# Kernel tuning notes

Hardware: AMD Instinct MI355X
Metric: run time of the kernel (lower is better)

Reference implementation:

```python
import jax, jax.numpy as jnp
import numpy as np

N = 50000      # nodes
E = 800000     # edges
FEAT = 128     # input feature dim
EMB = 256      # embed_dim = heads * hid
H = 4          # attention heads
C = 64         # hid_dim per head
PED = 32       # positional encoding dim
NEG_SLOPE = 0.2


def setup_inputs() -> dict:
    key = jax.random.key(0)
    ks = jax.random.split(key, 20)
    s = lambda i, shape, sc=0.1: jax.random.normal(ks[i], shape, jnp.float32) * sc
    return {
        "x": s(0, (N, FEAT), 1.0),
        "x_masked": s(1, (N, FEAT), 1.0),
        "PE": s(2, (N, PED), 1.0),
        "PE_noise": s(3, (N, PED), 1.0),
        "edge_index": jax.random.randint(ks[4], (2, E), 0, N),
        # PEG positional encoder (linear + relu)
        "W_peg": s(5, (PED, PED)), "b_peg": jnp.zeros((PED,), jnp.float32),
        # GAT layer 0
        "W0": s(6, (FEAT, H * C)), "a_s0": s(7, (H, C)), "a_d0": s(8, (H, C)),
        "w_pe0": s(9, (H,)), "W_u0": s(10, (PED, PED)),
        # GAT layer 1
        "W1": s(11, (EMB, H * C)), "a_s1": s(12, (H, C)), "a_d1": s(13, (H, C)),
        "w_pe1": s(14, (H,)), "W_u1": s(15, (PED, PED)),
    }


def _gat(x, pe, src, dst, W, a_s, a_d, w_pe, W_u):
    # PE-aware GATConv: standard GAT attention + PE-distance bias per head.
    xp = (x @ W).reshape(-1, H, C)                       # [N,H,C]
    al_s = (xp * a_s).sum(-1)                            # [N,H]
    al_d = (xp * a_d).sum(-1)                            # [N,H]
    dist = jnp.sqrt(((pe[src] - pe[dst]) ** 2).sum(-1) + 1e-8)   # [E]
    logits = jax.nn.leaky_relu(al_s[src] + al_d[dst], NEG_SLOPE) \
             + dist[:, None] * w_pe                      # [E,H]
    # segment softmax over incoming edges of each dst node
    m = jax.ops.segment_max(logits, dst, num_segments=N)
    e = jnp.exp(logits - m[dst])
    den = jax.ops.segment_sum(e, dst, num_segments=N)
    alpha = e / (den[dst] + 1e-16)                       # [E,H]
    out = jax.ops.segment_sum(alpha[:, :, None] * xp[src], dst,
                              num_segments=N).reshape(-1, H * C)  # [N,H*C]
    pe_out = jax.nn.relu(pe @ W_u)                       # per-layer PE update
    return out, pe_out


def reference(x, x_masked, PE, PE_noise, W_peg, b_peg,
              W0, a_s0, a_d0, w_pe0, W_u0,
              W1, a_s1, a_d1, w_pe1, W_u1, edge_index):
    src, dst = edge_index[0], edge_index[1]
    # PEG encoder on both PE branches
    pe = jax.nn.relu(PE @ W_peg + b_peg)
    pe_n = jax.nn.relu(PE_noise @ W_peg + b_peg)
    # layer 0 (dual branches; eval mode -> dropout is identity)
    h, pe_n = _gat(x, pe_n, src, dst, W0, a_s0, a_d0, w_pe0, W_u0)
    hm, pe = _gat(x_masked, pe, src, dst, W0, a_s0, a_d0, w_pe0, W_u0)
    h = jax.nn.relu(h)
    hm = jax.nn.relu(hm)
    # layer 1 (last layer: no activation)
    h, pe_n = _gat(h, pe_n, src, dst, W1, a_s1, a_d1, w_pe1, W_u1)
    hm, pe = _gat(hm, pe, src, dst, W1, a_s1, a_d1, w_pe1, W_u1)
    return (hm, pe_n)
```

## Files before the change

### kernel.cpp

```cpp
#include <hip/hip_runtime.h>
#include <hip/hip_bf16.h>

#define N_NODES 50000
#define N_EDGES 800000
#define NEG_SLOPE 0.2f

typedef __hip_bfloat16 bf16;
typedef __attribute__((ext_vector_type(8))) short short8;
typedef __attribute__((ext_vector_type(4))) float f32x4;
typedef __attribute__((ext_vector_type(2))) float f32x2;

__device__ __forceinline__ float b2f(bf16 x) { return __bfloat162float(x); }

__device__ __forceinline__ float ldsel(const void* p, size_t i, int isbf) {
  return isbf ? __bfloat162float(((const bf16*)p)[i]) : ((const float*)p)[i];
}
__device__ __forceinline__ void stsel(void* p, size_t i, int isbf, float v) {
  if (isbf) ((bf16*)p)[i] = __float2bfloat16(v);
  else ((float*)p)[i] = v;
}

__device__ __forceinline__ int block_detect(const unsigned short* __restrict__ probe) {
  __shared__ int wcount;
  int tid = threadIdx.x;
  if (tid == 0) wcount = 0;
  __syncthreads();
  int ex = (probe[2 * tid] >> 7) & 0xFF;
  unsigned long long m = __ballot(ex >= 0x85);
  if ((tid & 63) == 0) atomicAdd(&wcount, __popcll(m));
  __syncthreads();
  return wcount < 8;
}

struct CvtJobs {
  const void* src[10];
  float* dst[10];
  int n[10];
};
__global__ __launch_bounds__(256) void prep_kernel(CvtJobs jobs,
                                                   const unsigned short* __restrict__ probe,
                                                   const void* __restrict__ W0in,
                                                   bf16* __restrict__ Wt0,
                                                   const void* __restrict__ W1in,
                                                   bf16* __restrict__ Wt1,
                                                   int* __restrict__ flag,
                                                   const int* __restrict__ dst,
                                                   int* __restrict__ deg) {
  int tid = threadIdx.x;
  int b = blockIdx.x;
  if (b >= 400) {
    int e = (b - 400) * 256 + tid;
    atomicAdd(&deg[dst[e]], 1);
    return;
  }
  int isbf = block_detect(probe);
  if (b == 0 && tid == 0) *flag = isbf;
  if (b < 16) {
    for (int j = 0; j < 10; j++) {
      int n = jobs.n[j];
      const void* s = jobs.src[j];
      float* d = jobs.dst[j];
      for (int i = b * 256 + tid; i < n; i += 16 * 256) d[i] = ldsel(s, i, isbf);
    }
  } else if (b < 16 + 128) {
    int i = (b - 16) * 256 + tid;
    int n = i >> 7, k = i & 127;
    Wt0[i] = __float2bfloat16(ldsel(W0in, (size_t)k * 256 + n, isbf));
  } else {
    int i = (b - 144) * 256 + tid;
    int n = i >> 8, k = i & 255;
    Wt1[i] = __float2bfloat16(ldsel(W1in, (size_t)k * 256 + n, isbf));
  }
}

__global__ __launch_bounds__(1024) void scan_kernel(const int* __restrict__ deg,
                                                    int* __restrict__ rowptr,
                                                    int* __restrict__ bsum,
                                                    int* __restrict__ flags, int n) {
  __shared__ int wsum[16];
  __shared__ int spre;
  int tid = threadIdx.x;
  int idx = blockIdx.x * 1024 + tid;
  int v = (idx < n) ? deg[idx] : 0;
  int incl = v;
#pragma unroll
  for (int off = 1; off < 64; off <<= 1) {
    int t = __shfl_up(incl, off);
    if ((tid & 63) >= off) incl += t;
  }
  int wid = tid >> 6;
  if ((tid & 63) == 63) wsum[wid] = incl;
  __syncthreads();
  if (tid == 0) {
    int acc = 0;
#pragma unroll
    for (int w = 0; w < 16; w++) {
      int t = wsum[w];
      wsum[w] = acc;
      acc += t;
    }
    atomicExch(&bsum[blockIdx.x], acc);
    if (atomicAdd(&flags[0], 1) == 48) {
      int a = 0;
      for (int j = 0; j < 49; j++) {
        int t = atomicAdd(&bsum[j], 0);
        atomicExch(&bsum[j], a);
        a += t;
      }
      atomicExch(&flags[1], 1);
    }
    while (atomicAdd(&flags[1], 0) == 0) {}
    spre = atomicAdd(&bsum[blockIdx.x], 0);
  }
  __syncthreads();
  if (idx < n) rowptr[idx + 1] = spre + wsum[wid] + incl;
  if (idx == 0) rowptr[0] = 0;
}

#define NCHUNK (N_EDGES / 256)
#define NFILL8 (NCHUNK * 8)
#define NDIV8 (N_NODES / 8)
__global__ __launch_bounds__(256) void fill_peg_kernel(const int* __restrict__ src,
                                                       const int* __restrict__ dst,
                                                       const int* __restrict__ rowptr,
                                                       int* __restrict__ fill,
                                                       int* __restrict__ csr_src,
                                                       const void* __restrict__ pen,
                                                       const void* __restrict__ pem,
                                                       const float* __restrict__ Wpeg,
                                                       const float* __restrict__ bpeg,
                                                       const float* __restrict__ Wu0,
                                                       const float* __restrict__ Wu1,
                                                       void* out, size_t out_off,
                                                       char* __restrict__ blob0,
                                                       char* __restrict__ blob1,
                                                       const int* __restrict__ flag) {
  __shared__ float w1[1024], w2[1024], w3[1024];
  __shared__ float rowA[256], rowB[256];
  int tid = threadIdx.x;
  int b = blockIdx.x;
  if (b < NFILL8) {
    int xcd = b & 7;
    int e = (b >> 3) * 256 + tid;
    int d = dst[e];
    int lo = xcd * NDIV8;
    if (d >= lo && d < lo + NDIV8) {
      int pos = atomicAdd(&fill[d], 1);
      csr_src[rowptr[d] + pos] = src[e];
    }
    return;
  }
  int pb = b - NFILL8;
  int isbf = *flag;
  bool c3 = pb < NDIV8;
  int n0 = (c3 ? pb : pb - NDIV8) * 8;
  const void* in = c3 ? pen : pem;
  for (int i = tid; i < 1024; i += 256) {
    w1[i] = Wpeg[i];
    w2[i] = Wu0[i];
    if (c3) w3[i] = Wu1[i];
  }
  rowA[tid] = ldsel(in, (size_t)n0 * 32 + tid, isbf);
  __syncthreads();
  int col = tid & 31, ln = tid >> 5;
  size_t bi = ((size_t)(n0 + ln)) * 64 + col;
  float acc = bpeg[col];
#pragma unroll
  for (int j = 0; j < 32; j++) acc += rowA[ln * 32 + j] * w1[j * 32 + col];
  acc = fmaxf(acc, 0.f);
  if (!c3) ((bf16*)blob0)[bi] = __float2bfloat16(acc);
  rowB[tid] = acc;
  __syncthreads();
  acc = 0.f;
#pragma unroll
  for (int j = 0; j < 32; j++) acc += rowB[ln * 32 + j] * w2[j * 32 + col];
  acc = fmaxf(acc, 0.f);
  if (!c3) {
    ((bf16*)blob1)[bi] = __float2bfloat16(acc);
    return;
  }
  rowA[tid] = acc;
  __syncthreads();
  acc = 0.f;
#pragma unroll
  for (int j = 0; j < 32; j++) acc += rowA[ln * 32 + j] * w3[j * 32 + col];
  stsel(out, out_off + (size_t)n0 * 32 + tid, isbf, fmaxf(acc, 0.f));
}

template <int K, bool A_DUAL>
__global__ __launch_bounds__(256) void mfma_gemm(const void* __restrict__ Ap,
                                                 const bf16* __restrict__ Bt,
                                                 bf16* __restrict__ C, int M,
                                                 const float* __restrict__ a_sf,
                                                 const float* __restrict__ a_df,
                                                 char* __restrict__ blob,
                                                 float* __restrict__ al_d,
                                                 const int* __restrict__ flag) {
  constexpr int LDK = 136;
  __shared__ short a_lds[64 * LDK];
  __shared__ short b_lds[64 * LDK];
  __shared__ float lds_al[128];
  int nrt = (M + 63) / 64;
  int bid = blockIdx.x;
  int xcd = bid & 7;
  int jj = bid >> 3;
  int col_t = jj & 3;
  int row_t = (jj >> 2) * 8 + xcd;
  if (row_t >= nrt) return;
  int isbf = A_DUAL ? *flag : 1;
  int tid = threadIdx.x;
  int row0 = row_t * 64;
  int col0 = col_t * 64;
  int lane = tid & 63;
  int wv = tid >> 6;
  int wm = (wv & 1) * 32, wn = (wv >> 1) * 32;
  int l15 = lane & 15, quad = lane >> 4;
  if (tid < 128) lds_al[tid] = 0.f;
  f32x4 acc00 = {0.f, 0.f, 0.f, 0.f}, acc01 = acc00, acc10 = acc00, acc11 = acc00;

  for (int kb = 0; kb < K; kb += 128) {
    if (kb) __syncthreads();
    for (int idx = tid; idx < 64 * 16; idx += 256) {
      int r = idx >> 4, sidx = idx & 15;
      int gr = row0 + r;
      size_t gi = (size_t)gr * K + kb + sidx * 8;
      uint4 av = make_uint4(0u, 0u, 0u, 0u);
      if (A_DUAL && !isbf) {
        if (gr < M) {
          float4 f0 = ((const float4*)Ap)[gi / 4];
          float4 f1 = ((const float4*)Ap)[gi / 4 + 1];
          union { uint4 v; bf16 h[8]; } o;
          o.h[0] = __float2bfloat16(f0.x);
          o.h[1] = __float2bfloat16(f0.y);
          o.h[2] = __float2bfloat16(f0.z);
          o.h[3] = __float2bfloat16(f0.w);
          o.h[4] = __float2bfloat16(f1.x);
          o.h[5] = __float2bfloat16(f1.y);
          o.h[6] = __float2bfloat16(f1.z);
          o.h[7] = __float2bfloat16(f1.w);
          av = o.v;
        }
      } else {
        if (gr < M) av = *(const uint4*)&((const bf16*)Ap)[gi];
      }
      *(uint4*)&a_lds[r * LDK + sidx * 8] = av;
      *(uint4*)&b_lds[r * LDK + sidx * 8] =
          *(const uint4*)&Bt[(size_t)(col0 + r) * K + kb + sidx * 8];
    }
    __syncthreads();
#pragma unroll
    for (int k0 = 0; k0 < 128; k0 += 32) {
      int ko = k0 + quad * 8;
      short8 a0 = *(const short8*)&a_lds[(wm + l15) * LDK + ko];
      short8 a1 = *(const short8*)&a_lds[(wm + 16 + l15) * LDK + ko];
      short8 b0 = *(const short8*)&b_lds[(wn + l15) * LDK + ko];
      short8 b1 = *(const short8*)&b_lds[(wn + 16 + l15) * LDK + ko];
      acc00 = __builtin_amdgcn_mfma_f32_16x16x32_bf16(a0, b0, acc00, 0, 0, 0);
      acc01 = __builtin_amdgcn_mfma_f32_16x16x32_bf16(a0, b1, acc01, 0, 0, 0);
      acc10 = __builtin_amdgcn_mfma_f32_16x16x32_bf16(a1, b0, acc10, 0, 0, 0);
      acc11 = __builtin_amdgcn_mfma_f32_16x16x32_bf16(a1, b1, acc11, 0, 0, 0);
    }
  }
  const f32x4* accs[2][2] = {{&acc00, &acc01}, {&acc10, &acc11}};
  float as0 = a_sf[col0 + wn + l15], as1 = a_sf[col0 + wn + 16 + l15];
  float ad0 = a_df[col0 + wn + l15], ad1 = a_df[col0 + wn + 16 + l15];
#pragma unroll
  for (int i = 0; i < 2; i++) {
    float sp[4], dp[4];
#pragma unroll
    for (int r = 0; r < 4; r++) {
      float v0 = (*accs[i][0])[r], v1 = (*accs[i][1])[r];
      sp[r] = v0 * as0 + v1 * as1;
      dp[r] = v0 * ad0 + v1 * ad1;
      int grow = row0 + wm + i * 16 + quad * 4 + r;
      if (grow < M) {
        C[(size_t)grow * 256 + col0 + wn + l15] = __float2bfloat16(v0);
        C[(size_t)grow * 256 + col0 + wn + 16 + l15] = __float2bfloat16(v1);
      }
    }
#pragma unroll
    for (int off = 1; off < 16; off <<= 1) {
#pragma unroll
      for (int r = 0; r < 4; r++) {
        sp[r] += __shfl_xor(sp[r], off);
        dp[r] += __shfl_xor(dp[r], off);
      }
    }
    if (l15 == 0) {
#pragma unroll
      for (int r = 0; r < 4; r++) {
        int lrow = wm + i * 16 + quad * 4 + r;
        atomicAdd(&lds_al[lrow], sp[r]);
        atomicAdd(&lds_al[64 + lrow], dp[r]);
      }
    }
  }
  __syncthreads();
  if (tid < 64 && row0 + tid < M) {
    int row = row0 + tid;
    *(float*)(blob + (size_t)row * 128 + 64 + (size_t)col_t * 4) = lds_al[tid];
    al_d[(size_t)row * 4 + col_t] = lds_al[64 + tid];
  }
}

template <bool RELU, bool OUT_DUAL>
__global__ __launch_bounds__(256) void agg_kernel(const bf16* __restrict__ xp,
                                                  const char* __restrict__ blob,
                                                  const float* __restrict__ al_d,
                                                  const float* __restrict__ w_pe,
                                                  const int* __restrict__ csr_src,
                                                  const int* __restrict__ rowptr,
                                                  void* out, const int* __restrict__ flag) {
  int isbf = OUT_DUAL ? *flag : 1;
  int lane = threadIdx.x & 63;
  int n = blockIdx.x * 4 + (threadIdx.x >> 6);
  int q = lane >> 4, li = lane & 15, h = li >> 2;
  const char* bn = blob + (size_t)n * 128;
  unsigned int ud = *(const unsigned int*)(bn + li * 4);
  float pdlo = __uint_as_float(ud << 16);
  float pdhi = __uint_as_float(ud & 0xffff0000u);
  float ald = al_d[(size_t)n * 4 + h];
  float wph = w_pe[h];
  int s1 = rowptr[n + 1];
  int s = rowptr[n] + q;
  f32x2 acc2[8];
#pragma unroll
  for (int j = 0; j < 8; j++) acc2[j] = (f32x2){0.f, 0.f};
  float asum = 0.f;

  int sn_c = -1, sn_n = -1;
  unsigned int pes_c = 0, pes_n = 0;
  float als_c = 0.f, als_n = 0.f;
  uint4 z = make_uint4(0u, 0u, 0u, 0u);
  uint4 xc0 = z, xc1 = z, xn0 = z, xn1 = z;
  if (s < s1) {
    sn_c = csr_src[s];
    const char* bs = blob + (size_t)sn_c * 128;
    pes_c = *(const unsigned int*)(bs + li * 4);
    als_c = *(const float*)(bs + 64 + h * 4);
    const uint4* b = (const uint4*)&xp[(size_t)sn_c * 256 + li * 16];
    xc0 = b[0];
    xc1 = b[1];
    if (s + 4 < s1) sn_n = csr_src[s + 4];
  }
  int sf = s + 8;
  while (sn_c >= 0) {
    if (sn_n >= 0) {
      const char* bs = blob + (size_t)sn_n * 128;
      pes_n = *(const unsigned int*)(bs + li * 4);
      als_n = *(const float*)(bs + 64 + h * 4);
      const uint4* b = (const uint4*)&xp[(size_t)sn_n * 256 + li * 16];
      xn0 = b[0];
      xn1 = b[1];
    }
    int sn_f = (sf < s1) ? csr_src[sf] : -1;
    sf += 4;
    float dx = __uint_as_float(pes_c << 16) - pdlo;
    float dy = __uint_as_float(pes_c & 0xffff0000u) - pdhi;
    float d2 = dx * dx + dy * dy;
#pragma unroll
    for (int off = 1; off < 16; off <<= 1) d2 += __shfl_xor(d2, off);
    float lg = als_c + ald;
    lg = fmaxf(lg, 0.f) + NEG_SLOPE * fminf(lg, 0.f);
    lg += __builtin_amdgcn_sqrtf(d2 + 1e-8f) * wph;
    float a = __expf(lg);
    f32x2 av = {a, a};
    unsigned int u[8] = {xc0.x, xc0.y, xc0.z, xc0.w, xc1.x, xc1.y, xc1.z, xc1.w};
#pragma unroll
    for (int p = 0; p < 8; p++) {
      f32x2 xv;
      xv.x = __uint_as_float(u[p] << 16);
      xv.y = __uint_as_float(u[p] & 0xffff0000u);
      acc2[p] += av * xv;
    }
    asum += a;
    sn_c = sn_n;
    pes_c = pes_n;
    als_c = als_n;
    xc0 = xn0;
    xc1 = xn1;
    sn_n = sn_f;
  }
#pragma unroll
  for (int j = 0; j < 8; j++) {
    acc2[j].x += __shfl_xor(acc2[j].x, 16);
    acc2[j].x += __shfl_xor(acc2[j].x, 32);
    acc2[j].y += __shfl_xor(acc2[j].y, 16);
    acc2[j].y += __shfl_xor(acc2[j].y, 32);
  }
  asum += __shfl_xor(asum, 16);
  asum += __shfl_xor(asum, 32);
  if (q == 0) {
    float inv = 1.f / (asum + 1e-16f);
    size_t oi = (size_t)n * 256 + li * 16;
    if (OUT_DUAL && !isbf) {
      float* of = (float*)out;
#pragma unroll
      for (int p = 0; p < 4; p++) {
        float4 f;
        f.x = acc2[2 * p].x * inv;
        f.y = acc2[2 * p].y * inv;
        f.z = acc2[2 * p + 1].x * inv;
        f.w = acc2[2 * p + 1].y * inv;
        if (RELU) {
          f.x = fmaxf(f.x, 0.f);
          f.y = fmaxf(f.y, 0.f);
          f.z = fmaxf(f.z, 0.f);
          f.w = fmaxf(f.w, 0.f);
        }
        *(float4*)&of[oi + 4 * p] = f;
      }
    } else {
      union { uint4 v[2]; bf16 hh[16]; } o;
#pragma unroll
      for (int j = 0; j < 8; j++) {
        float rlo = acc2[j].x * inv;
        float rhi = acc2[j].y * inv;
        if (RELU) {
          rlo = fmaxf(rlo, 0.f);
          rhi = fmaxf(rhi, 0.f);
        }
        o.hh[2 * j] = __float2bfloat16(rlo);
        o.hh[2 * j + 1] = __float2bfloat16(rhi);
      }
      uint4* ob = (uint4*)&((bf16*)out)[oi];
      ob[0] = o.v[0];
      ob[1] = o.v[1];
    }
  }
}

extern "C" void kernel_launch(void* const* d_in, const int* in_sizes, int n_in,
                              void* d_out, int out_size, void* d_ws, size_t ws_size,
                              hipStream_t stream) {
  const void* x_masked = d_in[1];
  const void* PE = d_in[2];
  const void* PE_noise = d_in[3];
  const int* ei = (const int*)d_in[4];
  const int* src = ei;
  const int* dst = ei + N_EDGES;

  char* w = (char*)d_ws;
  auto alloc = [&](size_t bytes) -> char* {
    char* p = w;
    w += (bytes + 255) / 256 * 256;
    return p;
  };
  int* flag = (int*)alloc(4);
  float* W_peg_f = (float*)alloc(1024 * 4);
  float* b_peg_f = (float*)alloc(32 * 4);
  float* a_s0_f = (float*)alloc(256 * 4);
  float* a_d0_f = (float*)alloc(256 * 4);
  float* w_pe0_f = (float*)alloc(4 * 4);
  float* W_u0_f = (float*)alloc(1024 * 4);
  float* a_s1_f = (float*)alloc(256 * 4);
  float* a_d1_f = (float*)alloc(256 * 4);
  float* w_pe1_f = (float*)alloc(4 * 4);
  float* W_u1_f = (float*)alloc(1024 * 4);
  bf16* Wt0 = (bf16*)alloc(32768 * 2);
  bf16* Wt1 = (bf16*)alloc(65536 * 2);
  char* blob0 = alloc((size_t)N_NODES * 128);
  char* blob1 = alloc((size_t)N_NODES * 128);
  float* al_d = (float*)alloc((size_t)N_NODES * 4 * 4);
  int* degfill = (int*)alloc(((size_t)N_NODES * 2 + 64) * 4);
  int* deg = degfill;
  int* fill = degfill + N_NODES;
  int* sflags = degfill + 2 * N_NODES;
  int* rowptr = (int*)alloc((size_t)(N_NODES + 1) * 4);
  int* bsum = (int*)alloc(64 * 4);
  int* csr_src = (int*)alloc((size_t)N_EDGES * 4);
  bf16* xp = (bf16*)alloc((size_t)N_NODES * 256 * 2);
  bf16* hm0 = (bf16*)alloc((size_t)N_NODES * 256 * 2);

  CvtJobs jobs;
  int ji = 0;
  auto addjob = [&](const void* s, float* d, int n) {
    jobs.src[ji] = s; jobs.dst[ji] = d; jobs.n[ji] = n; ji++;
  };
  addjob(d_in[5], W_peg_f, 1024);
  addjob(d_in[6], b_peg_f, 32);
  addjob(d_in[8], a_s0_f, 256);
  addjob(d_in[9], a_d0_f, 256);
  addjob(d_in[10], w_pe0_f, 4);
  addjob(d_in[11], W_u0_f, 1024);
  addjob(d_in[13], a_s1_f, 256);
  addjob(d_in[14], a_d1_f, 256);
  addjob(d_in[15], w_pe1_f, 4);
  addjob(d_in[16], W_u1_f, 1024);

  hipMemsetAsync(degfill, 0, ((size_t)N_NODES * 2 + 64) * 4, stream);

  prep_kernel<<<400 + NCHUNK, 256, 0, stream>>>(
      jobs, (const unsigned short*)d_in[5], d_in[7], Wt0, d_in[12], Wt1, flag,
      dst, deg);

  scan_kernel<<<49, 1024, 0, stream>>>(deg, rowptr, bsum, sflags, N_NODES);

  fill_peg_kernel<<<NFILL8 + 2 * NDIV8, 256, 0, stream>>>(
      src, dst, rowptr, fill, csr_src, PE_noise, PE, W_peg_f, b_peg_f, W_u0_f,
      W_u1_f, d_out, (size_t)N_NODES * 256, blob0, blob1, flag);

  int nrt = (N_NODES + 63) / 64;
  int gblk = ((nrt + 7) / 8) * 8 * 4;

  mfma_gemm<128, true><<<gblk, 256, 0, stream>>>(x_masked, Wt0, xp, N_NODES,
                                                 a_s0_f, a_d0_f, blob0, al_d, flag);
  agg_kernel<true, false><<<N_NODES / 4, 256, 0, stream>>>(
      xp, blob0, al_d, w_pe0_f, csr_src, rowptr, hm0, flag);

  mfma_gemm<256, false><<<gblk, 256, 0, stream>>>(hm0, Wt1, xp, N_NODES,
                                                  a_s1_f, a_d1_f, blob1, al_d, flag);
  agg_kernel<false, true><<<N_NODES / 4, 256, 0, stream>>>(
      xp, blob1, al_d, w_pe1_f, csr_src, rowptr, d_out, flag);
}
```

Before: 453.4 us.

## Record edge slot during degree count and split scan into two kernels

The degree-counting pass now saves the atomicAdd return value per edge as that edge's slot within its destination row. The CSR fill pass can then write directly at rowptr+slot, with no second atomic pass over a fill array. The single-kernel scan, which used a spin-wait on a global flag for the cross-block prefix, is replaced by two kernels: a local scan that writes block sums, and a second that adds each block's prefix. The cost is an extra 3.2MB epos array, one more kernel launch, and an extra pass over a temporary array.

```diff
diff --git a/kernel.cpp b/kernel.cpp
--- a/kernel.cpp
+++ b/kernel.cpp
@@ -45,12 +45,13 @@
                                                    bf16* __restrict__ Wt1,
                                                    int* __restrict__ flag,
                                                    const int* __restrict__ dst,
-                                                   int* __restrict__ deg) {
+                                                   int* __restrict__ deg,
+                                                   int* __restrict__ epos) {
   int tid = threadIdx.x;
   int b = blockIdx.x;
   if (b >= 400) {
     int e = (b - 400) * 256 + tid;
-    atomicAdd(&deg[dst[e]], 1);
+    epos[e] = atomicAdd(&deg[dst[e]], 1);
     return;
   }
   int isbf = block_detect(probe);
@@ -73,12 +74,10 @@
   }
 }
 
-__global__ __launch_bounds__(1024) void scan_kernel(const int* __restrict__ deg,
-                                                    int* __restrict__ rowptr,
-                                                    int* __restrict__ bsum,
-                                                    int* __restrict__ flags, int n) {
+__global__ __launch_bounds__(1024) void scan1_kernel(const int* __restrict__ deg,
+                                                     int* __restrict__ tmp,
+                                                     int* __restrict__ bsum, int n) {
   __shared__ int wsum[16];
-  __shared__ int spre;
   int tid = threadIdx.x;
   int idx = blockIdx.x * 1024 + tid;
   int v = (idx < n) ? deg[idx] : 0;
@@ -99,21 +98,24 @@
       wsum[w] = acc;
       acc += t;
     }
-    atomicExch(&bsum[blockIdx.x], acc);
-    if (atomicAdd(&flags[0], 1) == 48) {
-      int a = 0;
-      for (int j = 0; j < 49; j++) {
-        int t = atomicAdd(&bsum[j], 0);
-        atomicExch(&bsum[j], a);
-        a += t;
-      }
-      atomicExch(&flags[1], 1);
-    }
-    while (atomicAdd(&flags[1], 0) == 0) {}
-    spre = atomicAdd(&bsum[blockIdx.x], 0);
-  }
-  __syncthreads();
-  if (idx < n) rowptr[idx + 1] = spre + wsum[wid] + incl;
+    bsum[blockIdx.x] = acc;
+  }
+  __syncthreads();
+  if (idx < n) tmp[idx] = wsum[wid] + incl;
+}
+
+__global__ __launch_bounds__(1024) void scan3_kernel(const int* __restrict__ tmp,
+                                                     const int* __restrict__ bsum,
+                                                     int* __restrict__ rowptr, int n,
+                                                     int nb) {
+  __shared__ int lb[64];
+  int tid = threadIdx.x;
+  if (tid < nb) lb[tid] = bsum[tid];
+  __syncthreads();
+  int pre = 0;
+  for (int j = 0; j < blockIdx.x; j++) pre += lb[j];
+  int idx = blockIdx.x * 1024 + tid;
+  if (idx < n) rowptr[idx + 1] = tmp[idx] + pre;
   if (idx == 0) rowptr[0] = 0;
 }
 
@@ -123,7 +125,7 @@
 __global__ __launch_bounds__(256) void fill_peg_kernel(const int* __restrict__ src,
                                                        const int* __restrict__ dst,
                                                        const int* __restrict__ rowptr,
-                                                       int* __restrict__ fill,
+                                                       const int* __restrict__ epos,
                                                        int* __restrict__ csr_src,
                                                        const void* __restrict__ pen,
                                                        const void* __restrict__ pem,
@@ -145,8 +147,7 @@
     int d = dst[e];
     int lo = xcd * NDIV8;
     if (d >= lo && d < lo + NDIV8) {
-      int pos = atomicAdd(&fill[d], 1);
-      csr_src[rowptr[d] + pos] = src[e];
+      csr_src[rowptr[d] + epos[e]] = src[e];
     }
     return;
   }
@@ -462,11 +463,10 @@
   char* blob0 = alloc((size_t)N_NODES * 128);
   char* blob1 = alloc((size_t)N_NODES * 128);
   float* al_d = (float*)alloc((size_t)N_NODES * 4 * 4);
-  int* degfill = (int*)alloc(((size_t)N_NODES * 2 + 64) * 4);
-  int* deg = degfill;
-  int* fill = degfill + N_NODES;
-  int* sflags = degfill + 2 * N_NODES;
+  int* deg = (int*)alloc((size_t)N_NODES * 4);
+  int* epos = (int*)alloc((size_t)N_EDGES * 4);
   int* rowptr = (int*)alloc((size_t)(N_NODES + 1) * 4);
+  int* stmp = (int*)alloc((size_t)N_NODES * 4);
   int* bsum = (int*)alloc(64 * 4);
   int* csr_src = (int*)alloc((size_t)N_EDGES * 4);
   bf16* xp = (bf16*)alloc((size_t)N_NODES * 256 * 2);
@@ -488,16 +488,17 @@
   addjob(d_in[15], w_pe1_f, 4);
   addjob(d_in[16], W_u1_f, 1024);
 
-  hipMemsetAsync(degfill, 0, ((size_t)N_NODES * 2 + 64) * 4, stream);
+  hipMemsetAsync(deg, 0, (size_t)N_NODES * 4, stream);
 
   prep_kernel<<<400 + NCHUNK, 256, 0, stream>>>(
       jobs, (const unsigned short*)d_in[5], d_in[7], Wt0, d_in[12], Wt1, flag,
-      dst, deg);
-
-  scan_kernel<<<49, 1024, 0, stream>>>(deg, rowptr, bsum, sflags, N_NODES);
+      dst, deg, epos);
+
+  scan1_kernel<<<49, 1024, 0, stream>>>(deg, stmp, bsum, N_NODES);
+  scan3_kernel<<<49, 1024, 0, stream>>>(stmp, bsum, rowptr, N_NODES, 49);
 
   fill_peg_kernel<<<NFILL8 + 2 * NDIV8, 256, 0, stream>>>(
-      src, dst, rowptr, fill, csr_src, PE_noise, PE, W_peg_f, b_peg_f, W_u0_f,
+      src, dst, rowptr, epos, csr_src, PE_noise, PE, W_peg_f, b_peg_f, W_u0_f,
       W_u1_f, d_out, (size_t)N_NODES * 256, blob0, blob1, flag);
 
   int nrt = (N_NODES + 63) / 64;
```

New measurement: 408.5 us. 9.9% less time.
